# Kernel optimization log

Hardware: AMD Instinct MI355X
Metric: run time of the kernel (lower is better)

Reference implementation:

```python
import jax, jax.numpy as jnp
import numpy as np

N_CLOUDS = 16
N_PTS = 2048
K = 5            # spline kernel_size per dim
KC = K ** 3      # 125 kernel weights
BITS = np.array([[i & 1, (i >> 1) & 1, (i >> 2) & 1] for i in range(8)])  # degree-1 B-spline corners


def _radius_edges_np(pos, batch, r, max_nb=32):
    # brute-force radius graph, up to max_nb nearest neighbors within r, no self loops
    srcs, tgts = [], []
    for c in np.unique(batch):
        ids = np.where(batch == c)[0]
        P = pos[ids]
        D = np.linalg.norm(P[:, None, :] - P[None, :, :], axis=-1).astype(np.float32)
        np.fill_diagonal(D, np.inf)
        D[D > r] = np.inf
        order = np.argsort(D, axis=1)[:, :max_nb]
        valid = np.isfinite(np.take_along_axis(D, order, axis=1))
        tgt_loc = np.broadcast_to(np.arange(len(ids))[:, None], order.shape)
        srcs.append(ids[order[valid]])
        tgts.append(ids[tgt_loc[valid]])
    return np.concatenate(srcs).astype(np.int32), np.concatenate(tgts).astype(np.int32)


def _fps_np(pos, batch, ratio):
    out = []
    for c in np.unique(batch):
        ids = np.where(batch == c)[0]
        P = pos[ids]
        m = int(round(ratio * len(ids)))
        sel = [0]
        d = np.linalg.norm(P - P[0], axis=1)
        for _ in range(m - 1):
            i = int(d.argmax())
            sel.append(i)
            d = np.minimum(d, np.linalg.norm(P - P[i], axis=1))
        out.append(ids[np.array(sel)])
    return np.concatenate(out).astype(np.int32)


def setup_inputs() -> dict:
    rng = np.random.default_rng(0)
    pos = rng.random((N_CLOUDS * N_PTS, 3)).astype(np.float32)
    batch = np.repeat(np.arange(N_CLOUDS), N_PTS).astype(np.int32)

    src1, tgt1 = _radius_edges_np(pos, batch, 0.2)
    idx1 = _fps_np(pos, batch, 0.5)
    pos2, batch2 = pos[idx1], batch[idx1]
    src2, tgt2 = _radius_edges_np(pos2, batch2, 0.4)
    idx2 = _fps_np(pos2, batch2, 0.25)
    pos3, batch3 = pos2[idx2], batch2[idx2]
    src3, tgt3 = _radius_edges_np(pos3, batch3, 1.0)

    def p(shape, scale=0.1):
        return (rng.standard_normal(shape) * scale).astype(np.float32)

    inp = {
        'pos': jnp.asarray(pos), 'batch': jnp.asarray(batch),
        'src1': jnp.asarray(src1), 'tgt1': jnp.asarray(tgt1),
        'src2': jnp.asarray(src2), 'tgt2': jnp.asarray(tgt2),
        'src3': jnp.asarray(src3), 'tgt3': jnp.asarray(tgt3),
        'idx1': jnp.asarray(idx1), 'idx2': jnp.asarray(idx2),
        'W1': jnp.asarray(p((KC, 1, 64))),  'R1': jnp.asarray(p((1, 64))),   'b1': jnp.zeros((64,), jnp.float32),
        'W2': jnp.asarray(p((KC, 64, 64))), 'R2': jnp.asarray(p((64, 64))),  'b2': jnp.zeros((64,), jnp.float32),
        'W3': jnp.asarray(p((KC, 64, 128))),'R3': jnp.asarray(p((64, 128))), 'b3': jnp.zeros((128,), jnp.float32),
        'lw1': jnp.asarray(p((128, 256))), 'lb1': jnp.zeros((256,), jnp.float32),
        'lw2': jnp.asarray(p((256, 256))), 'lb2': jnp.zeros((256,), jnp.float32),
        'lw3': jnp.asarray(p((256, 10))),  'lb3': jnp.zeros((10,), jnp.float32),
    }
    return inp


def _pseudo(pos, src, tgt, r):
    return jnp.clip((pos[tgt] - pos[src]) / (2.0 * r) + 0.5, 0.0, 1.0)


def _spline_conv(x, pseudo, src, tgt, n, W, R, b):
    # SplineConv: degree-1 open B-spline basis, mean aggregation, root weight + bias
    Cin = x.shape[1]
    v = pseudo * (K - 1)                  # [E,3]
    bot = jnp.floor(v)
    frac = v - bot                        # [E,3]
    boti = bot.astype(jnp.int32)
    xj = x[src]                           # [E,Cin]
    A = jnp.zeros((n * KC, Cin), x.dtype)
    for s in range(8):                    # 8 nonzero basis products per edge
        bits = BITS[s]
        w = jnp.where(bits == 1, frac, 1.0 - frac).prod(-1)     # [E]
        idx = jnp.clip(boti + bits, 0, K - 1)                   # [E,3]
        wi = idx[:, 0] + K * idx[:, 1] + K * K * idx[:, 2]      # [E]
        A = A.at[tgt * KC + wi].add(w[:, None] * xj)
    A = A.reshape(n, KC, Cin)             # per-node per-kernel accumulated features
    msg = jnp.einsum('nkc,kco->no', A, W)
    deg = jax.ops.segment_sum(jnp.ones(tgt.shape[0], x.dtype), tgt, num_segments=n)
    msg = msg / jnp.maximum(deg, 1.0)[:, None]
    return msg + x @ R + b


def reference(pos, batch, src1, tgt1, src2, tgt2, src3, tgt3, idx1, idx2,
              W1, R1, b1, W2, R2, b2, W3, R3, b3,
              lw1, lb1, lw2, lb2, lw3, lb3):
    n1 = pos.shape[0]
    x = jnp.ones((n1, 1), pos.dtype)
    x = jax.nn.elu(_spline_conv(x, _pseudo(pos, src1, tgt1, 0.2), src1, tgt1, n1, W1, R1, b1))
    x, pos2 = x[idx1], pos[idx1]
    n2 = pos2.shape[0]
    x = jax.nn.elu(_spline_conv(x, _pseudo(pos2, src2, tgt2, 0.4), src2, tgt2, n2, W2, R2, b2))
    x, pos3 = x[idx2], pos2[idx2]
    n3 = pos3.shape[0]
    x = jax.nn.elu(_spline_conv(x, _pseudo(pos3, src3, tgt3, 1.0), src3, tgt3, n3, W3, R3, b3))
    batch3 = batch[idx1][idx2]
    num = jax.ops.segment_sum(x, batch3, num_segments=N_CLOUDS)
    cnt = jax.ops.segment_sum(jnp.ones(n3, x.dtype), batch3, num_segments=N_CLOUDS)
    g = num / jnp.maximum(cnt, 1.0)[:, None]          # global_mean_pool [16,128]
    h = jax.nn.elu(g @ lw1 + lb1)
    h = jax.nn.elu(h @ lw2 + lb2)
    # dropout is identity in eval mode
    logits = h @ lw3 + lb3
    return jax.nn.log_softmax(logits, axis=-1)
```

## Files before the change

### kernel.cpp

```cpp
#include <hip/hip_runtime.h>
#include <hip/hip_bf16.h>
#include <math.h>

#define KDIM 5
#define KC 125
#define KPAD 8192
#define EPB 32
#define NSPLIT 4
#define LDA 72
#define SSTR 40
#define XSTR 40
#define H1STR 40
#define MAXCHUNK 8192

typedef short bf16x8 __attribute__((ext_vector_type(8)));
typedef float f32x4 __attribute__((ext_vector_type(4)));

__device__ __forceinline__ float elu_f(float x) { return x > 0.f ? x : (expf(x) - 1.f); }

__device__ __forceinline__ void fadd_atomic(float* p, float v) {
    unsafeAtomicAdd(p, v);
}

__device__ __forceinline__ unsigned short f2bf(float x) {
    union { float f; unsigned u; } v; v.f = x;
    unsigned r = (v.u + 0x7FFFu + ((v.u >> 16) & 1u)) >> 16;
    return (unsigned short)r;
}

__global__ void rowptr_kernel(const int* __restrict__ tgt, int E, int n, int* __restrict__ rowptr)
{
    int e = blockIdx.x * blockDim.x + threadIdx.x;
    if (e > E) return;
    if (e < E) {
        int t = tgt[e];
        int p = (e == 0) ? -1 : tgt[e - 1];
        for (int v = p + 1; v <= t; v++) rowptr[v] = e;
    } else {
        int p = tgt[E - 1];
        for (int v = p + 1; v <= n; v++) rowptr[v] = E;
    }
}

__global__ void slots_kernel(const float* __restrict__ posL, const int* __restrict__ src,
                             const int* __restrict__ tgt, int E, float rinv2, int sinkrow,
                             unsigned* __restrict__ slots)
{
    int e = blockIdx.x * blockDim.x + threadIdx.x;
    if (e >= E) return;
    int s = src[e], t = tgt[e];
    float p0 = fminf(fmaxf((posL[t*3+0] - posL[s*3+0]) * rinv2 + 0.5f, 0.f), 1.f);
    float p1 = fminf(fmaxf((posL[t*3+1] - posL[s*3+1]) * rinv2 + 0.5f, 0.f), 1.f);
    float p2 = fminf(fmaxf((posL[t*3+2] - posL[s*3+2]) * rinv2 + 0.5f, 0.f), 1.f);
    float v0 = p0 * (KDIM - 1), v1 = p1 * (KDIM - 1), v2 = p2 * (KDIM - 1);
    int b0 = (int)floorf(v0), b1 = (int)floorf(v1), b2 = (int)floorf(v2);
    float f0 = v0 - (float)b0, f1 = v1 - (float)b1, f2 = v2 - (float)b2;
    unsigned out[8];
    #pragma unroll
    for (int sb = 0; sb < 8; sb++) {
        int i0 = sb & 1, i1 = (sb >> 1) & 1, i2 = (sb >> 2) & 1;
        float w = (i0 ? f0 : 1.f - f0) * (i1 ? f1 : 1.f - f1) * (i2 ? f2 : 1.f - f2);
        int k0 = min(b0 + i0, KDIM - 1), k1 = min(b1 + i1, KDIM - 1), k2 = min(b2 + i2, KDIM - 1);
        int wi = k0 + KDIM * k1 + KDIM * KDIM * k2;
        if (w == 0.f) wi = sinkrow;
        out[sb] = (__float_as_uint(w) & ~127u) | (unsigned)wi;
    }
    uint4* dst = (uint4*)&slots[(size_t)e * 8];
    dst[0] = make_uint4(out[0], out[1], out[2], out[3]);
    dst[1] = make_uint4(out[4], out[5], out[6], out[7]);
}

__global__ __launch_bounds__(256) void histo1_kernel(const unsigned* __restrict__ slots,
                                                     const int* __restrict__ rowptr,
                                                     unsigned short* __restrict__ Aout)
{
    __shared__ __attribute__((aligned(16))) unsigned short S[4][128 * H1STR];
    int wave = threadIdx.x >> 6, lane = threadIdx.x & 63;
    int node = blockIdx.x * 4 + wave;
    int rs = rowptr[node], re = rowptr[node + 1];
    int deg = re - rs;
    unsigned short* Sw = S[wave];

    for (int i = lane; i < 128 * H1STR / 8; i += 64)
        ((uint4*)Sw)[i] = make_uint4(0, 0, 0, 0);

    int wbase = lane * 4;
    if (wbase < deg * 8) {
        uint4 sw = *(const uint4*)&slots[(size_t)rs * 8 + wbase];
        unsigned wd[4] = {sw.x, sw.y, sw.z, sw.w};
        #pragma unroll
        for (int j = 0; j < 4; j++) {
            int e = (wbase + j) >> 3;
            int wi = wd[j] & 127u;
            Sw[wi * H1STR + e] = f2bf(__uint_as_float(wd[j] & ~127u));
        }
    }
    __syncthreads();

    const short one = 0x3F80;
    bf16x8 bones = {one, one, one, one, one, one, one, one};
    int fr = lane & 15, fq = (lane >> 4) * 8;
    f32x4 acc[8];
    #pragma unroll
    for (int tl = 0; tl < 8; tl++) {
        bf16x8 af = *(const bf16x8*)&Sw[(tl * 16 + fr) * H1STR + fq];
        acc[tl] = __builtin_amdgcn_mfma_f32_16x16x32_bf16(
            af, bones, (f32x4){0.f, 0.f, 0.f, 0.f}, 0, 0, 0);
    }

    float invdeg = 1.f / fmaxf((float)deg, 1.f);
    if ((lane & 15) == 0) {
        int rbase = (lane >> 4) * 4;
        #pragma unroll
        for (int tl = 0; tl < 8; tl++)
            #pragma unroll
            for (int r = 0; r < 4; r++) {
                int row = tl * 16 + rbase + r;
                float v = (row < KC) ? acc[tl][r] * invdeg : (row == KC ? 1.f : 0.f);
                Sw[row] = f2bf(v);
            }
    }
    __syncthreads();
    unsigned lo = Sw[2 * lane], hi = Sw[2 * lane + 1];
    ((unsigned*)(Aout + (size_t)node * 128))[lane] = lo | (hi << 16);
}

__global__ __launch_bounds__(256) void buildA_kernel(
    const unsigned* __restrict__ slots, const int* __restrict__ src,
    const int* __restrict__ rowptr, const unsigned short* __restrict__ xbf,
    int nodeBase, unsigned short* __restrict__ Aout)
{
    __shared__ __attribute__((aligned(16))) unsigned short BUF[8192];
    __shared__ int Es[EPB];
    unsigned short* S  = BUF;
    unsigned short* XT = BUF + 128 * SSTR;
    int node = nodeBase + blockIdx.x;
    int t = threadIdx.x;
    int rs = rowptr[node], re = rowptr[node + 1];
    int ne = re - rs;
    int wave = t >> 6, lane = t & 63;
    int fr = lane & 15, fq = (lane >> 4) * 8;
    int quad = lane >> 4;

    for (int i = t; i < (128 * SSTR + 64 * XSTR) / 8; i += 256)
        ((uint4*)BUF)[i] = make_uint4(0, 0, 0, 0);
    if (t < ne) Es[t] = src[rs + t];
    __syncthreads();
    if (t < ne * 8) {
        int e = t >> 3;
        unsigned word = slots[(size_t)rs * 8 + t];
        int wi = word & 127u;
        S[wi * SSTR + e] = f2bf(__uint_as_float(word & ~127u));
    }
    for (int i = t; i < ne * 64; i += 256) {
        int c = i & 63, el = i >> 6;
        XT[c * XSTR + el] = xbf[(size_t)Es[el] * 64 + c];
    }
    __syncthreads();

    f32x4 acc[2][4];
    #pragma unroll
    for (int i = 0; i < 2; i++)
        #pragma unroll
        for (int j = 0; j < 4; j++) acc[i][j] = (f32x4){0.f, 0.f, 0.f, 0.f};
    #pragma unroll
    for (int i = 0; i < 2; i++) {
        bf16x8 af = *(const bf16x8*)&S[((2 * wave + i) * 16 + fr) * SSTR + fq];
        #pragma unroll
        for (int j = 0; j < 4; j++) {
            bf16x8 bg = *(const bf16x8*)&XT[(j * 16 + fr) * XSTR + fq];
            acc[i][j] = __builtin_amdgcn_mfma_f32_16x16x32_bf16(af, bg, acc[i][j], 0, 0, 0);
        }
    }
    __syncthreads();

    float invdeg = 1.f / fmaxf((float)ne, 1.f);
    #pragma unroll
    for (int i = 0; i < 2; i++) {
        int wibase = (2 * wave + i) * 16 + quad * 4;
        #pragma unroll
        for (int r = 0; r < 4; r++) {
            int wi = wibase + r;
            if (wi < KC) {
                #pragma unroll
                for (int j = 0; j < 4; j++)
                    BUF[wi * 64 + j * 16 + fr] = f2bf(acc[i][j][r] * invdeg);
            }
        }
    }
    if (t < 64) BUF[8000 + t] = xbf[(size_t)node * 64 + t];
    else if (t < 192) BUF[8000 + t] = 0;
    __syncthreads();

    uint4* out4 = (uint4*)(Aout + (size_t)blockIdx.x * KPAD);
    const uint4* b4 = (const uint4*)BUF;
    #pragma unroll
    for (int k = 0; k < 4; k++) out4[t + k * 256] = b4[t + k * 256];
}

__global__ void concatWT_kernel(const float* __restrict__ W, const float* __restrict__ R,
                                int COUT, int kpad, int krows, int cin,
                                unsigned short* __restrict__ WfT)
{
    int i = blockIdx.x * blockDim.x + threadIdx.x;
    if (i >= COUT * kpad) return;
    int n = i / kpad, k = i - n * kpad;
    float v = 0.f;
    if (k < krows) v = W[(size_t)k * COUT + n];
    else if (k < krows + cin) v = R[(size_t)(k - krows) * COUT + n];
    WfT[i] = f2bf(v);
}

__global__ __launch_bounds__(256) void gemm_kernel(const unsigned short* __restrict__ A,
                                                   const unsigned short* __restrict__ BT,
                                                   int Mrows, int COUT, int Ksz, int lda,
                                                   float* __restrict__ P)
{
    __shared__ __attribute__((aligned(16))) unsigned short As[2 * 64 * LDA];
    __shared__ __attribute__((aligned(16))) unsigned short Bs[2 * 64 * LDA];
    int t = threadIdx.x;
    int mblk = blockIdx.x * 64, nblk = blockIdx.y * 64;
    int kBase = blockIdx.z * Ksz;

    int lr = t >> 2;
    int lc = (t & 3) * 16;

    const unsigned short* Ap = A + (size_t)(mblk + lr) * lda + kBase + lc;
    const unsigned short* Bp = BT + (size_t)(nblk + lr) * lda + kBase + lc;

    uint4 a0 = *(const uint4*)Ap;  uint4 a1 = *(const uint4*)(Ap + 8);
    uint4 b0 = *(const uint4*)Bp;  uint4 b1 = *(const uint4*)(Bp + 8);

    int wave = t >> 6, lane = t & 63;
    int mw = (wave & 1) * 32, nw = (wave >> 1) * 32;
    int fr = lane & 15;
    int fq = (lane >> 4) * 8;

    f32x4 acc[2][2];
    #pragma unroll
    for (int i = 0; i < 2; i++)
        #pragma unroll
        for (int j = 0; j < 2; j++) acc[i][j] = (f32x4){0.f, 0.f, 0.f, 0.f};

    *(uint4*)&As[lr * LDA + lc]     = a0;
    *(uint4*)&As[lr * LDA + lc + 8] = a1;
    *(uint4*)&Bs[lr * LDA + lc]     = b0;
    *(uint4*)&Bs[lr * LDA + lc + 8] = b1;
    __syncthreads();

    int ktiles = Ksz / 64;
    for (int kt = 0; kt < ktiles; kt++) {
        int cur = (kt & 1) * 64 * LDA;
        if (kt + 1 < ktiles) {
            Ap += 64; Bp += 64;
            a0 = *(const uint4*)Ap; a1 = *(const uint4*)(Ap + 8);
            b0 = *(const uint4*)Bp; b1 = *(const uint4*)(Bp + 8);
        }
        #pragma unroll
        for (int ks = 0; ks < 2; ks++) {
            bf16x8 af0 = *(const bf16x8*)&As[cur + (mw + fr) * LDA + ks * 32 + fq];
            bf16x8 af1 = *(const bf16x8*)&As[cur + (mw + 16 + fr) * LDA + ks * 32 + fq];
            bf16x8 bg0 = *(const bf16x8*)&Bs[cur + (nw + fr) * LDA + ks * 32 + fq];
            bf16x8 bg1 = *(const bf16x8*)&Bs[cur + (nw + 16 + fr) * LDA + ks * 32 + fq];
            acc[0][0] = __builtin_amdgcn_mfma_f32_16x16x32_bf16(af0, bg0, acc[0][0], 0, 0, 0);
            acc[0][1] = __builtin_amdgcn_mfma_f32_16x16x32_bf16(af0, bg1, acc[0][1], 0, 0, 0);
            acc[1][0] = __builtin_amdgcn_mfma_f32_16x16x32_bf16(af1, bg0, acc[1][0], 0, 0, 0);
            acc[1][1] = __builtin_amdgcn_mfma_f32_16x16x32_bf16(af1, bg1, acc[1][1], 0, 0, 0);
        }
        if (kt + 1 < ktiles) {
            int nxt = ((kt + 1) & 1) * 64 * LDA;
            *(uint4*)&As[nxt + lr * LDA + lc]     = a0;
            *(uint4*)&As[nxt + lr * LDA + lc + 8] = a1;
            *(uint4*)&Bs[nxt + lr * LDA + lc]     = b0;
            *(uint4*)&Bs[nxt + lr * LDA + lc + 8] = b1;
        }
        __syncthreads();
    }
    float* Pz = P + (size_t)blockIdx.z * Mrows * COUT;
    int crow = (lane >> 4) * 4, ccol = lane & 15;
    #pragma unroll
    for (int i = 0; i < 2; i++)
        #pragma unroll
        for (int j = 0; j < 2; j++) {
            int m0 = mblk + mw + i * 16 + crow;
            int n0 = nblk + nw + j * 16 + ccol;
            #pragma unroll
            for (int r = 0; r < 4; r++)
                Pz[(size_t)(m0 + r) * COUT + n0] = acc[i][j][r];
        }
}

__global__ void combine_kernel(const float* __restrict__ P, const float* __restrict__ b,
                               int Mrows, int COUT, int NS, float* __restrict__ xout)
{
    int i = blockIdx.x * blockDim.x + threadIdx.x;
    int total = Mrows * COUT;
    if (i >= total) return;
    float s = 0.f;
    for (int z = 0; z < NS; z++) s += P[(size_t)z * total + i];
    int o = i % COUT;
    xout[i] = elu_f(s + b[o]);
}

__global__ void xgather_kernel(const float* __restrict__ x_src, const int* __restrict__ idx,
                               int n, unsigned short* __restrict__ x_dst)
{
    int tid = blockIdx.x * blockDim.x + threadIdx.x;
    if (tid >= n * 64) return;
    int i = tid >> 6, c = tid & 63;
    x_dst[tid] = f2bf(x_src[(size_t)idx[i] * 64 + c]);
}

__global__ void posgather_kernel(const float* __restrict__ pos_src, const int* __restrict__ idx,
                                 int n, float* __restrict__ pos_dst)
{
    int tid = blockIdx.x * blockDim.x + threadIdx.x;
    if (tid >= n * 3) return;
    int i = tid / 3, d = tid - i * 3;
    pos_dst[tid] = pos_src[idx[i] * 3 + d];
}

__global__ void zero_kernel(float* __restrict__ p, int n)
{
    int i = blockIdx.x * blockDim.x + threadIdx.x;
    if (i < n) p[i] = 0.f;
}

__global__ void cid_kernel(const int* __restrict__ batch, const int* __restrict__ idx1,
                           const int* __restrict__ idx2, int n3,
                           int* __restrict__ cid, float* __restrict__ cnt)
{
    __shared__ int h[16];
    int t = threadIdx.x;
    int i = blockIdx.x * 256 + t;
    if (t < 16) h[t] = 0;
    __syncthreads();
    if (i < n3) {
        int cl = batch[idx1[idx2[i]]];
        cid[i] = cl;
        atomicAdd(&h[cl], 1);
    }
    __syncthreads();
    if (t < 16 && h[t] > 0) fadd_atomic(&cnt[t], (float)h[t]);
}

__global__ void pool2_kernel(const float* __restrict__ x3, const int* __restrict__ cid,
                             int n3, float* __restrict__ gnum)
{
    int t = threadIdx.x;
    int c = t & 127, h = t >> 7;
    int base = blockIdx.x * 64;
    int nn = min(64, n3 - base);
    float sum = 0.f; int cur = -1;
    for (int j = h; j < nn; j += 2) {
        int i = base + j;
        int cl = cid[i];
        if (cl != cur) {
            if (cur >= 0) fadd_atomic(&gnum[cur * 128 + c], sum);
            cur = cl; sum = 0.f;
        }
        sum += x3[(size_t)i * 128 + c];
    }
    if (cur >= 0) fadd_atomic(&gnum[cur * 128 + c], sum);
}

__global__ void mlp_kernel(const float* __restrict__ gnum, const float* __restrict__ cnt,
                           const float* __restrict__ lw1, const float* __restrict__ lb1,
                           const float* __restrict__ lw2, const float* __restrict__ lb2,
                           const float* __restrict__ lw3, const float* __restrict__ lb3,
                           float* __restrict__ out)
{
    __shared__ float gv[128], h1[256], h2[256], lg[10];
    __shared__ float lse_s;
    int cl = blockIdx.x, t = threadIdx.x;
    if (t < 128) gv[t] = gnum[cl * 128 + t] / fmaxf(cnt[cl], 1.f);
    __syncthreads();
    float a = lb1[t];
    for (int c = 0; c < 128; c++) a += gv[c] * lw1[c * 256 + t];
    h1[t] = elu_f(a);
    __syncthreads();
    a = lb2[t];
    for (int c = 0; c < 256; c++) a += h1[c] * lw2[c * 256 + t];
    h2[t] = elu_f(a);
    __syncthreads();
    if (t < 10) {
        a = lb3[t];
        for (int c = 0; c < 256; c++) a += h2[c] * lw3[c * 10 + t];
        lg[t] = a;
    }
    __syncthreads();
    if (t == 0) {
        float m = -1e30f;
        for (int i = 0; i < 10; i++) m = fmaxf(m, lg[i]);
        float s = 0.f;
        for (int i = 0; i < 10; i++) s += expf(lg[i] - m);
        lse_s = m + logf(s);
    }
    __syncthreads();
    if (t < 10) out[cl * 10 + t] = lg[t] - lse_s;
}

static void run_level(const unsigned* slots, const int* src, const int* rowptr,
                      const unsigned short* xbf, const unsigned short* WfT, const float* bvec,
                      int n, int COUT, unsigned short* Abuf, int AbufRows, float* P,
                      float* xout, hipStream_t stream)
{
    int Ksz = KPAD / NSPLIT;
    for (int cs = 0; cs < n; cs += AbufRows) {
        int cr = min(AbufRows, n - cs);
        buildA_kernel<<<cr, 256, 0, stream>>>(slots, src, rowptr, xbf, cs, Abuf);
        dim3 grid(cr / 64, COUT / 64, NSPLIT);
        gemm_kernel<<<grid, 256, 0, stream>>>(Abuf, WfT, cr, COUT, Ksz, KPAD, P);
        combine_kernel<<<(cr * COUT + 255) / 256, 256, 0, stream>>>(P, bvec, cr, COUT, NSPLIT,
                                                                    xout + (size_t)cs * COUT);
    }
}

extern "C" void kernel_launch(void* const* d_in, const int* in_sizes, int n_in,
                              void* d_out, int out_size, void* d_ws, size_t ws_size,
                              hipStream_t stream)
{
    const float* pos   = (const float*)d_in[0];
    const int*   batch = (const int*)d_in[1];
    const int*   src1  = (const int*)d_in[2];
    const int*   tgt1  = (const int*)d_in[3];
    const int*   src2  = (const int*)d_in[4];
    const int*   tgt2  = (const int*)d_in[5];
    const int*   src3  = (const int*)d_in[6];
    const int*   tgt3  = (const int*)d_in[7];
    const int*   idx1  = (const int*)d_in[8];
    const int*   idx2  = (const int*)d_in[9];
    const float* W1 = (const float*)d_in[10];
    const float* R1 = (const float*)d_in[11];
    const float* b1 = (const float*)d_in[12];
    const float* W2 = (const float*)d_in[13];
    const float* R2 = (const float*)d_in[14];
    const float* b2 = (const float*)d_in[15];
    const float* W3 = (const float*)d_in[16];
    const float* R3 = (const float*)d_in[17];
    const float* b3 = (const float*)d_in[18];
    const float* lw1 = (const float*)d_in[19];
    const float* lb1 = (const float*)d_in[20];
    const float* lw2 = (const float*)d_in[21];
    const float* lb2 = (const float*)d_in[22];
    const float* lw3 = (const float*)d_in[23];
    const float* lb3 = (const float*)d_in[24];

    int n1 = in_sizes[0] / 3;
    int E1 = in_sizes[2];
    int E2 = in_sizes[4];
    int E3 = in_sizes[6];
    int n2 = in_sizes[8];
    int n3 = in_sizes[9];

    float* ws = (float*)d_ws;
    float* x1   = ws;
    float* x2o  = x1   + (size_t)n1 * 64;
    float* x3o  = x2o  + (size_t)n2 * 64;
    float* pos2 = x3o  + (size_t)n3 * 128;
    float* pos3 = pos2 + (size_t)n2 * 3;
    float* gnum = pos3 + (size_t)n3 * 3;
    float* cnt  = gnum + 16 * 128;
    int*   cid  = (int*)(cnt + 16);
    unsigned short* x2in = (unsigned short*)(cid + ((n3 + 4) & ~3));
    unsigned short* x3in = x2in + (size_t)n2 * 64;
    unsigned short* WfT1 = x3in + (size_t)n3 * 64;
    unsigned short* WfT2 = WfT1 + (size_t)64 * 128;
    unsigned short* WfT3 = WfT2 + (size_t)64 * KPAD;
    int*   rp1  = (int*)(WfT3 + (size_t)128 * KPAD);
    int*   rp2  = rp1 + ((n1 + 4) & ~3);
    int*   rp3  = rp2 + ((n2 + 4) & ~3);
    unsigned* slots1 = (unsigned*)(rp3 + ((n3 + 4) & ~3));
    unsigned* slots2 = slots1 + (size_t)E1 * 8;
    unsigned* slots3 = slots2 + (size_t)E2 * 8;
    unsigned short* A1buf = (unsigned short*)(slots3 + (size_t)E3 * 8);
    float*  P    = (float*)(A1buf + (size_t)n1 * 128);
    unsigned short* Abuf = (unsigned short*)(P + (size_t)8 * 1024 * 1024);

    size_t usedBytes = (size_t)((char*)Abuf - (char*)ws);
    size_t availBytes = ws_size > usedBytes ? ws_size - usedBytes : 0;
    int maxRows = (int)(availBytes / ((size_t)KPAD * 2));
    maxRows &= ~63;
    if (maxRows < 64) maxRows = 64;
    if (maxRows > MAXCHUNK) maxRows = MAXCHUNK;
    int rowsP2 = ((8 * 1024 * 1024) / (NSPLIT * 64)) & ~63;
    int rowsP3 = ((8 * 1024 * 1024) / (NSPLIT * 128)) & ~63;
    int rows2 = min(min(maxRows, rowsP2), n2);
    int rows3 = min(min(maxRows, rowsP3), n3);

    float* out = (float*)d_out;

    rowptr_kernel<<<(E1 + 256) / 256, 256, 0, stream>>>(tgt1, E1, n1, rp1);
    rowptr_kernel<<<(E2 + 256) / 256, 256, 0, stream>>>(tgt2, E2, n2, rp2);
    rowptr_kernel<<<(E3 + 256) / 256, 256, 0, stream>>>(tgt3, E3, n3, rp3);
    posgather_kernel<<<(n2 * 3 + 255) / 256, 256, 0, stream>>>(pos, idx1, n2, pos2);
    posgather_kernel<<<(n3 * 3 + 255) / 256, 256, 0, stream>>>(pos2, idx2, n3, pos3);
    slots_kernel<<<(E1 + 255) / 256, 256, 0, stream>>>(pos,  src1, tgt1, E1, 2.5f,  126, slots1);
    slots_kernel<<<(E2 + 255) / 256, 256, 0, stream>>>(pos2, src2, tgt2, E2, 1.25f, 125, slots2);
    slots_kernel<<<(E3 + 255) / 256, 256, 0, stream>>>(pos3, src3, tgt3, E3, 0.5f,  125, slots3);
    concatWT_kernel<<<(64 * 128 + 255) / 256, 256, 0, stream>>>(W1, R1, 64, 128, KC, 1, WfT1);
    concatWT_kernel<<<(64 * KPAD + 255) / 256, 256, 0, stream>>>(W2, R2, 64, KPAD, KC * 64, 64, WfT2);
    concatWT_kernel<<<(128 * KPAD + 255) / 256, 256, 0, stream>>>(W3, R3, 128, KPAD, KC * 64, 64, WfT3);

    zero_kernel<<<(16 * 128 + 16 + 255) / 256, 256, 0, stream>>>(gnum, 16 * 128 + 16);
    cid_kernel<<<(n3 + 255) / 256, 256, 0, stream>>>(batch, idx1, idx2, n3, cid, cnt);

    histo1_kernel<<<n1 / 4, 256, 0, stream>>>(slots1, rp1, A1buf);
    {
        dim3 g1(n1 / 64, 1, 1);
        gemm_kernel<<<g1, 256, 0, stream>>>(A1buf, WfT1, n1, 64, 128, 128, P);
        combine_kernel<<<(n1 * 64 + 255) / 256, 256, 0, stream>>>(P, b1, n1, 64, 1, x1);
    }
    xgather_kernel<<<(n2 * 64 + 255) / 256, 256, 0, stream>>>(x1, idx1, n2, x2in);

    run_level(slots2, src2, rp2, x2in, WfT2, b2, n2, 64, Abuf, rows2, P, x2o, stream);
    xgather_kernel<<<(n3 * 64 + 255) / 256, 256, 0, stream>>>(x2o, idx2, n3, x3in);

    run_level(slots3, src3, rp3, x3in, WfT3, b3, n3, 128, Abuf, rows3, P, x3o, stream);

    pool2_kernel<<<(n3 + 63) / 64, 256, 0, stream>>>(x3o, cid, n3, gnum);
    mlp_kernel<<<16, 256, 0, stream>>>(gnum, cnt, lw1, lb1, lw2, lb2, lw3, lb3, out);
}
```

Measured before the change: 395.4 us.

## Merge preprocessing kernels and fuse combine with gather and pooling

Collapses the rowptr, pos-gather, slots, weight-concat, zero and cluster-id launches into two flat-indexed kernels. Fuses the level-1 combine with the idx1 gather so the full x1 is never written, and fuses the level-3 combine with the global mean pooling through per-element atomics. This cuts launch count and intermediate global traffic. In exchange, per-element atomics into a 16x128 buffer may contend, and cid counting now uses one global atomic per node instead of a shared-memory histogram.

```diff
diff --git a/kernel.cpp b/kernel.cpp
--- a/kernel.cpp
+++ b/kernel.cpp
@@ -28,10 +28,9 @@
     return (unsigned short)r;
 }
 
-__global__ void rowptr_kernel(const int* __restrict__ tgt, int E, int n, int* __restrict__ rowptr)
-{
-    int e = blockIdx.x * blockDim.x + threadIdx.x;
-    if (e > E) return;
+__device__ __forceinline__ void rowptr_seg(const int* __restrict__ tgt, int E, int n,
+                                           int* __restrict__ rowptr, int e)
+{
     if (e < E) {
         int t = tgt[e];
         int p = (e == 0) ? -1 : tgt[e - 1];
@@ -42,12 +41,11 @@
     }
 }
 
-__global__ void slots_kernel(const float* __restrict__ posL, const int* __restrict__ src,
-                             const int* __restrict__ tgt, int E, float rinv2, int sinkrow,
-                             unsigned* __restrict__ slots)
-{
-    int e = blockIdx.x * blockDim.x + threadIdx.x;
-    if (e >= E) return;
+__device__ __forceinline__ void slots_seg(const float* __restrict__ posL,
+                                          const int* __restrict__ src,
+                                          const int* __restrict__ tgt, float rinv2,
+                                          int sinkrow, unsigned* __restrict__ slots, int e)
+{
     int s = src[e], t = tgt[e];
     float p0 = fminf(fmaxf((posL[t*3+0] - posL[s*3+0]) * rinv2 + 0.5f, 0.f), 1.f);
     float p1 = fminf(fmaxf((posL[t*3+1] - posL[s*3+1]) * rinv2 + 0.5f, 0.f), 1.f);
@@ -68,6 +66,72 @@
     uint4* dst = (uint4*)&slots[(size_t)e * 8];
     dst[0] = make_uint4(out[0], out[1], out[2], out[3]);
     dst[1] = make_uint4(out[4], out[5], out[6], out[7]);
+}
+
+__device__ __forceinline__ void concat_seg(const float* __restrict__ W,
+                                           const float* __restrict__ R,
+                                           int COUT, int kpad, int krows, int cin,
+                                           unsigned short* __restrict__ WfT, int i)
+{
+    int n = i / kpad, k = i - n * kpad;
+    float v = 0.f;
+    if (k < krows) v = W[(size_t)k * COUT + n];
+    else if (k < krows + cin) v = R[(size_t)(k - krows) * COUT + n];
+    WfT[i] = f2bf(v);
+}
+
+__global__ void pre1_kernel(const float* __restrict__ pos, const int* __restrict__ idx1,
+                            const int* __restrict__ idx2, int n2, int n3,
+                            float* __restrict__ pos2, float* __restrict__ pos3,
+                            float* __restrict__ gz )
+{
+    int i = blockIdx.x * blockDim.x + threadIdx.x;
+    int w0 = n2 * 3, w1 = w0 + n3 * 3, w2 = w1 + 16 * 128 + 16;
+    if (i < w0) {
+        int r = i / 3, d = i - r * 3;
+        pos2[i] = pos[idx1[r] * 3 + d];
+    } else if (i < w1) {
+        int j = i - w0;
+        int r = j / 3, d = j - r * 3;
+        pos3[j] = pos[idx1[idx2[r]] * 3 + d];
+    } else if (i < w2) {
+        gz[i - w1] = 0.f;
+    }
+}
+
+__global__ void pre2_kernel(
+    const int* __restrict__ tgt1, int E1, int n1, int* __restrict__ rp1,
+    const int* __restrict__ tgt2, int E2, int n2, int* __restrict__ rp2,
+    const int* __restrict__ tgt3, int E3, int n3, int* __restrict__ rp3,
+    const float* __restrict__ pos,  const int* __restrict__ src1, unsigned* __restrict__ slots1,
+    const float* __restrict__ pos2, const int* __restrict__ src2, unsigned* __restrict__ slots2,
+    const float* __restrict__ pos3, const int* __restrict__ src3, unsigned* __restrict__ slots3,
+    const float* __restrict__ W1, const float* __restrict__ R1, unsigned short* __restrict__ WfT1,
+    const float* __restrict__ W2, const float* __restrict__ R2, unsigned short* __restrict__ WfT2,
+    const float* __restrict__ W3, const float* __restrict__ R3, unsigned short* __restrict__ WfT3,
+    const int* __restrict__ batch, const int* __restrict__ idx1, const int* __restrict__ idx2,
+    int* __restrict__ cid, float* __restrict__ cnt)
+{
+    int i = blockIdx.x * blockDim.x + threadIdx.x;
+    int e0 = E1 + 1, e1 = e0 + E2 + 1, e2 = e1 + E3 + 1;
+    int e3 = e2 + E1, e4 = e3 + E2, e5 = e4 + E3;
+    int e6 = e5 + 64 * 128, e7 = e6 + 64 * KPAD, e8 = e7 + 128 * KPAD;
+    int e9 = e8 + n3;
+    if (i < e0)      rowptr_seg(tgt1, E1, n1, rp1, i);
+    else if (i < e1) rowptr_seg(tgt2, E2, n2, rp2, i - e0);
+    else if (i < e2) rowptr_seg(tgt3, E3, n3, rp3, i - e1);
+    else if (i < e3) slots_seg(pos,  src1, tgt1, 2.5f,  126, slots1, i - e2);
+    else if (i < e4) slots_seg(pos2, src2, tgt2, 1.25f, 125, slots2, i - e3);
+    else if (i < e5) slots_seg(pos3, src3, tgt3, 0.5f,  125, slots3, i - e4);
+    else if (i < e6) concat_seg(W1, R1, 64, 128, KC, 1, WfT1, i - e5);
+    else if (i < e7) concat_seg(W2, R2, 64, KPAD, KC * 64, 64, WfT2, i - e6);
+    else if (i < e8) concat_seg(W3, R3, 128, KPAD, KC * 64, 64, WfT3, i - e7);
+    else if (i < e9) {
+        int j = i - e8;
+        int cl = batch[idx1[idx2[j]]];
+        cid[j] = cl;
+        fadd_atomic(&cnt[cl], 1.f);
+    }
 }
 
 __global__ __launch_bounds__(256) void histo1_kernel(const unsigned* __restrict__ slots,
@@ -198,19 +262,6 @@
     for (int k = 0; k < 4; k++) out4[t + k * 256] = b4[t + k * 256];
 }
 
-__global__ void concatWT_kernel(const float* __restrict__ W, const float* __restrict__ R,
-                                int COUT, int kpad, int krows, int cin,
-                                unsigned short* __restrict__ WfT)
-{
-    int i = blockIdx.x * blockDim.x + threadIdx.x;
-    if (i >= COUT * kpad) return;
-    int n = i / kpad, k = i - n * kpad;
-    float v = 0.f;
-    if (k < krows) v = W[(size_t)k * COUT + n];
-    else if (k < krows + cin) v = R[(size_t)(k - krows) * COUT + n];
-    WfT[i] = f2bf(v);
-}
-
 __global__ __launch_bounds__(256) void gemm_kernel(const unsigned short* __restrict__ A,
                                                    const unsigned short* __restrict__ BT,
                                                    int Mrows, int COUT, int Ksz, int lda,
@@ -302,6 +353,30 @@
     xout[i] = elu_f(s + b[o]);
 }
 
+__global__ void combine1g_kernel(const float* __restrict__ P, const float* __restrict__ b,
+                                 const int* __restrict__ idx1, int n2,
+                                 unsigned short* __restrict__ x2in)
+{
+    int i = blockIdx.x * blockDim.x + threadIdx.x;
+    if (i >= n2 * 64) return;
+    int r = i >> 6, c = i & 63;
+    x2in[i] = f2bf(elu_f(P[(size_t)idx1[r] * 64 + c] + b[c]));
+}
+
+__global__ void combinepool_kernel(const float* __restrict__ P, const float* __restrict__ b,
+                                   const int* __restrict__ cid, int cs, int Mrows, int NS,
+                                   float* __restrict__ gnum)
+{
+    int i = blockIdx.x * blockDim.x + threadIdx.x;
+    int total = Mrows * 128;
+    if (i >= total) return;
+    int r = i >> 7, c = i & 127;
+    float s = 0.f;
+    for (int z = 0; z < NS; z++) s += P[(size_t)z * total + i];
+    float v = elu_f(s + b[c]);
+    fadd_atomic(&gnum[cid[cs + r] * 128 + c], v);
+}
+
 __global__ void xgather_kernel(const float* __restrict__ x_src, const int* __restrict__ idx,
                                int n, unsigned short* __restrict__ x_dst)
 {
@@ -309,59 +384,6 @@
     if (tid >= n * 64) return;
     int i = tid >> 6, c = tid & 63;
     x_dst[tid] = f2bf(x_src[(size_t)idx[i] * 64 + c]);
-}
-
-__global__ void posgather_kernel(const float* __restrict__ pos_src, const int* __restrict__ idx,
-                                 int n, float* __restrict__ pos_dst)
-{
-    int tid = blockIdx.x * blockDim.x + threadIdx.x;
-    if (tid >= n * 3) return;
-    int i = tid / 3, d = tid - i * 3;
-    pos_dst[tid] = pos_src[idx[i] * 3 + d];
-}
-
-__global__ void zero_kernel(float* __restrict__ p, int n)
-{
-    int i = blockIdx.x * blockDim.x + threadIdx.x;
-    if (i < n) p[i] = 0.f;
-}
-
-__global__ void cid_kernel(const int* __restrict__ batch, const int* __restrict__ idx1,
-                           const int* __restrict__ idx2, int n3,
-                           int* __restrict__ cid, float* __restrict__ cnt)
-{
-    __shared__ int h[16];
-    int t = threadIdx.x;
-    int i = blockIdx.x * 256 + t;
-    if (t < 16) h[t] = 0;
-    __syncthreads();
-    if (i < n3) {
-        int cl = batch[idx1[idx2[i]]];
-        cid[i] = cl;
-        atomicAdd(&h[cl], 1);
-    }
-    __syncthreads();
-    if (t < 16 && h[t] > 0) fadd_atomic(&cnt[t], (float)h[t]);
-}
-
-__global__ void pool2_kernel(const float* __restrict__ x3, const int* __restrict__ cid,
-                             int n3, float* __restrict__ gnum)
-{
-    int t = threadIdx.x;
-    int c = t & 127, h = t >> 7;
-    int base = blockIdx.x * 64;
-    int nn = min(64, n3 - base);
-    float sum = 0.f; int cur = -1;
-    for (int j = h; j < nn; j += 2) {
-        int i = base + j;
-        int cl = cid[i];
-        if (cl != cur) {
-            if (cur >= 0) fadd_atomic(&gnum[cur * 128 + c], sum);
-            cur = cl; sum = 0.f;
-        }
-        sum += x3[(size_t)i * 128 + c];
-    }
-    if (cur >= 0) fadd_atomic(&gnum[cur * 128 + c], sum);
 }
 
 __global__ void mlp_kernel(const float* __restrict__ gnum, const float* __restrict__ cnt,
@@ -398,22 +420,6 @@
     }
     __syncthreads();
     if (t < 10) out[cl * 10 + t] = lg[t] - lse_s;
-}
-
-static void run_level(const unsigned* slots, const int* src, const int* rowptr,
-                      const unsigned short* xbf, const unsigned short* WfT, const float* bvec,
-                      int n, int COUT, unsigned short* Abuf, int AbufRows, float* P,
-                      float* xout, hipStream_t stream)
-{
-    int Ksz = KPAD / NSPLIT;
-    for (int cs = 0; cs < n; cs += AbufRows) {
-        int cr = min(AbufRows, n - cs);
-        buildA_kernel<<<cr, 256, 0, stream>>>(slots, src, rowptr, xbf, cs, Abuf);
-        dim3 grid(cr / 64, COUT / 64, NSPLIT);
-        gemm_kernel<<<grid, 256, 0, stream>>>(Abuf, WfT, cr, COUT, Ksz, KPAD, P);
-        combine_kernel<<<(cr * COUT + 255) / 256, 256, 0, stream>>>(P, bvec, cr, COUT, NSPLIT,
-                                                                    xout + (size_t)cs * COUT);
-    }
 }
 
 extern "C" void kernel_launch(void* const* d_in, const int* in_sizes, int n_in,
@@ -454,10 +460,8 @@
     int n3 = in_sizes[9];
 
     float* ws = (float*)d_ws;
-    float* x1   = ws;
-    float* x2o  = x1   + (size_t)n1 * 64;
-    float* x3o  = x2o  + (size_t)n2 * 64;
-    float* pos2 = x3o  + (size_t)n3 * 128;
+    float* x2o  = ws;
+    float* pos2 = x2o  + (size_t)n2 * 64;
     float* pos3 = pos2 + (size_t)n2 * 3;
     float* gnum = pos3 + (size_t)n3 * 3;
     float* cnt  = gnum + 16 * 128;
@@ -489,35 +493,46 @@
     int rows3 = min(min(maxRows, rowsP3), n3);
 
     float* out = (float*)d_out;
-
-    rowptr_kernel<<<(E1 + 256) / 256, 256, 0, stream>>>(tgt1, E1, n1, rp1);
-    rowptr_kernel<<<(E2 + 256) / 256, 256, 0, stream>>>(tgt2, E2, n2, rp2);
-    rowptr_kernel<<<(E3 + 256) / 256, 256, 0, stream>>>(tgt3, E3, n3, rp3);
-    posgather_kernel<<<(n2 * 3 + 255) / 256, 256, 0, stream>>>(pos, idx1, n2, pos2);
-    posgather_kernel<<<(n3 * 3 + 255) / 256, 256, 0, stream>>>(pos2, idx2, n3, pos3);
-    slots_kernel<<<(E1 + 255) / 256, 256, 0, stream>>>(pos,  src1, tgt1, E1, 2.5f,  126, slots1);
-    slots_kernel<<<(E2 + 255) / 256, 256, 0, stream>>>(pos2, src2, tgt2, E2, 1.25f, 125, slots2);
-    slots_kernel<<<(E3 + 255) / 256, 256, 0, stream>>>(pos3, src3, tgt3, E3, 0.5f,  125, slots3);
-    concatWT_kernel<<<(64 * 128 + 255) / 256, 256, 0, stream>>>(W1, R1, 64, 128, KC, 1, WfT1);
-    concatWT_kernel<<<(64 * KPAD + 255) / 256, 256, 0, stream>>>(W2, R2, 64, KPAD, KC * 64, 64, WfT2);
-    concatWT_kernel<<<(128 * KPAD + 255) / 256, 256, 0, stream>>>(W3, R3, 128, KPAD, KC * 64, 64, WfT3);
-
-    zero_kernel<<<(16 * 128 + 16 + 255) / 256, 256, 0, stream>>>(gnum, 16 * 128 + 16);
-    cid_kernel<<<(n3 + 255) / 256, 256, 0, stream>>>(batch, idx1, idx2, n3, cid, cnt);
+    int Ksz = KPAD / NSPLIT;
+
+    {
+        int tot1 = n2 * 3 + n3 * 3 + 16 * 128 + 16;
+        pre1_kernel<<<(tot1 + 255) / 256, 256, 0, stream>>>(pos, idx1, idx2, n2, n3,
+                                                            pos2, pos3, gnum);
+        int tot2 = (E1 + 1) + (E2 + 1) + (E3 + 1) + E1 + E2 + E3
+                 + 64 * 128 + 64 * KPAD + 128 * KPAD + n3;
+        pre2_kernel<<<(tot2 + 255) / 256, 256, 0, stream>>>(
+            tgt1, E1, n1, rp1, tgt2, E2, n2, rp2, tgt3, E3, n3, rp3,
+            pos,  src1, slots1, pos2, src2, slots2, pos3, src3, slots3,
+            W1, R1, WfT1, W2, R2, WfT2, W3, R3, WfT3,
+            batch, idx1, idx2, cid, cnt);
+    }
 
     histo1_kernel<<<n1 / 4, 256, 0, stream>>>(slots1, rp1, A1buf);
     {
         dim3 g1(n1 / 64, 1, 1);
         gemm_kernel<<<g1, 256, 0, stream>>>(A1buf, WfT1, n1, 64, 128, 128, P);
-        combine_kernel<<<(n1 * 64 + 255) / 256, 256, 0, stream>>>(P, b1, n1, 64, 1, x1);
-    }
-    xgather_kernel<<<(n2 * 64 + 255) / 256, 256, 0, stream>>>(x1, idx1, n2, x2in);
-
-    run_level(slots2, src2, rp2, x2in, WfT2, b2, n2, 64, Abuf, rows2, P, x2o, stream);
+        combine1g_kernel<<<(n2 * 64 + 255) / 256, 256, 0, stream>>>(P, b1, idx1, n2, x2in);
+    }
+
+    for (int cs = 0; cs < n2; cs += rows2) {
+        int cr = min(rows2, n2 - cs);
+        buildA_kernel<<<cr, 256, 0, stream>>>(slots2, src2, rp2, x2in, cs, Abuf);
+        dim3 grid(cr / 64, 1, NSPLIT);
+        gemm_kernel<<<grid, 256, 0, stream>>>(Abuf, WfT2, cr, 64, Ksz, KPAD, P);
+        combine_kernel<<<(cr * 64 + 255) / 256, 256, 0, stream>>>(P, b2, cr, 64, NSPLIT,
+                                                                  x2o + (size_t)cs * 64);
+    }
     xgather_kernel<<<(n3 * 64 + 255) / 256, 256, 0, stream>>>(x2o, idx2, n3, x3in);
 
-    run_level(slots3, src3, rp3, x3in, WfT3, b3, n3, 128, Abuf, rows3, P, x3o, stream);
-
-    pool2_kernel<<<(n3 + 63) / 64, 256, 0, stream>>>(x3o, cid, n3, gnum);
+    for (int cs = 0; cs < n3; cs += rows3) {
+        int cr = min(rows3, n3 - cs);
+        buildA_kernel<<<cr, 256, 0, stream>>>(slots3, src3, rp3, x3in, cs, Abuf);
+        dim3 grid(cr / 64, 2, NSPLIT);
+        gemm_kernel<<<grid, 256, 0, stream>>>(Abuf, WfT3, cr, 128, Ksz, KPAD, P);
+        combinepool_kernel<<<(cr * 128 + 255) / 256, 256, 0, stream>>>(P, b3, cid, cs, cr,
+                                                                       NSPLIT, gnum);
+    }
+
     mlp_kernel<<<16, 256, 0, stream>>>(gnum, cnt, lw1, lb1, lw2, lb2, lw3, lb3, out);
 }
```

Result: no change. 400.4 us (+1.3%).
